# Kernel tuning notes

Hardware: AMD Instinct MI355X
Metric: run time of the kernel (lower is better)

Reference implementation:

```python
import jax, jax.numpy as jnp
import numpy as np

IN_CH = 1024
EMB = 1024
OUT = 768


def setup_inputs() -> dict:
    key = jax.random.key(0)
    ks = jax.random.split(key, 12)
    B, S = 8, 2048
    std = 1.0 / np.sqrt(IN_CH)
    return {
        "image_embeds": jax.random.normal(ks[0], (B, S, IN_CH), jnp.float32),
        "ref_pose_embeds": jax.random.normal(ks[1], (B, S, IN_CH), jnp.float32),
        "pose_embeds": jax.random.normal(ks[2], (B, S, IN_CH), jnp.float32),
        "ln_gamma": jnp.ones((IN_CH,), jnp.float32),
        "ln_beta": jnp.zeros((IN_CH,), jnp.float32),
        "Wq": jax.random.normal(ks[3], (EMB, IN_CH), jnp.float32) * std,
        "bq": jnp.zeros((EMB,), jnp.float32),
        "Wk": jax.random.normal(ks[4], (EMB, IN_CH), jnp.float32) * std,
        "bk": jnp.zeros((EMB,), jnp.float32),
        "Wv": jax.random.normal(ks[5], (EMB, IN_CH), jnp.float32) * std,
        "bv": jnp.zeros((EMB,), jnp.float32),
        "Wo": jax.random.normal(ks[6], (OUT, EMB), jnp.float32) * (1.0 / np.sqrt(EMB)),
        "bo": jnp.zeros((OUT,), jnp.float32),
    }


def _layernorm(x, gamma, beta, eps=1e-5):
    mu = jnp.mean(x, axis=-1, keepdims=True)
    var = jnp.var(x, axis=-1, keepdims=True)
    return (x - mu) * jax.lax.rsqrt(var + eps) * gamma + beta


def reference(image_embeds, ref_pose_embeds, pose_embeds,
              ln_gamma, ln_beta, Wq, bq, Wk, bk, Wv, bv, Wo, bo):
    scale = EMB ** (-0.5)
    # shared LayerNorm applied to all three streams (as in original)
    img_n = _layernorm(image_embeds, ln_gamma, ln_beta)
    ref_n = _layernorm(ref_pose_embeds, ln_gamma, ln_beta)
    pose_n = _layernorm(pose_embeds, ln_gamma, ln_beta)
    Q = ref_n @ Wq.T + bq   # [B,S,E]
    K = pose_n @ Wk.T + bk
    V = img_n @ Wv.T + bv
    att = jnp.einsum('bid,bjd->bij', Q, K) * scale  # [B,S,S]
    att = jax.nn.softmax(att, axis=-1)
    out = jnp.einsum('bij,bjd->bid', att, V)
    out = out + pose_n + img_n
    return out @ Wo.T + bo  # [B,S,768]
```

## Files before the change

### kernel.cpp

```cpp
#include <hip/hip_runtime.h>
#include <hip/hip_bf16.h>
#include <hip/hip_fp16.h>

typedef __attribute__((ext_vector_type(8))) short short8;
typedef __attribute__((ext_vector_type(4))) float f32x4;
typedef unsigned short u16;

__device__ __forceinline__ u16 f2bf(float f) {
  union { float f; unsigned u; } v; v.f = f;
  unsigned r = v.u + 0x7fffu + ((v.u >> 16) & 1u);
  return (u16)(r >> 16);
}
__device__ __forceinline__ float bf2f(u16 u) {
  union { unsigned u; float f; } v; v.u = ((unsigned)u) << 16;
  return v.f;
}
__device__ __forceinline__ u16 f2h(float f) {
  __half h = __float2half(f);
  union { __half h; u16 u; } v; v.h = h;
  return v.u;
}
__device__ __forceinline__ void gload16(const void* g, void* l) {
  __builtin_amdgcn_global_load_lds(
      (const __attribute__((address_space(1))) unsigned*)g,
      (__attribute__((address_space(3))) unsigned*)l, 16, 0, 0);
}

#define FENCE asm volatile("" ::: "memory")
#define SB0 __builtin_amdgcn_sched_barrier(0)

__global__ __launch_bounds__(256)
void ln3(const float* __restrict__ refp, const float* __restrict__ pose,
         const float* __restrict__ img, const float* __restrict__ gamma,
         const float* __restrict__ beta, u16* __restrict__ oA,
         u16* __restrict__ oB, u16* __restrict__ oC) {
  const int row = blockIdx.x;
  const int tid = threadIdx.x;
  const float* X = (blockIdx.y == 0) ? refp : (blockIdx.y == 1) ? pose : img;
  u16* Y = (blockIdx.y == 0) ? oA : (blockIdx.y == 1) ? oB : oC;
  const long base = (long)row * 1024 + tid * 4;
  float4 x = *(const float4*)(X + base);
  float s = x.x + x.y + x.z + x.w;
  float q = x.x * x.x + x.y * x.y + x.z * x.z + x.w * x.w;
#pragma unroll
  for (int o = 32; o > 0; o >>= 1) {
    s += __shfl_xor(s, o);
    q += __shfl_xor(q, o);
  }
  __shared__ float rs[4], rq[4];
  if ((tid & 63) == 0) { rs[tid >> 6] = s; rq[tid >> 6] = q; }
  __syncthreads();
  s = rs[0] + rs[1] + rs[2] + rs[3];
  q = rq[0] + rq[1] + rq[2] + rq[3];
  float mu = s * (1.f / 1024.f);
  float var = q * (1.f / 1024.f) - mu * mu;
  float rstd = rsqrtf(var + 1e-5f);
  float4 g = *(const float4*)(gamma + tid * 4);
  float4 b = *(const float4*)(beta + tid * 4);
  ushort4 o4;
  o4.x = f2bf((x.x - mu) * rstd * g.x + b.x);
  o4.y = f2bf((x.y - mu) * rstd * g.y + b.y);
  o4.z = f2bf((x.z - mu) * rstd * g.z + b.z);
  o4.w = f2bf((x.w - mu) * rstd * g.w + b.w);
  *(ushort4*)(Y + base) = o4;
}

__global__ __launch_bounds__(256)
void cvt_all(const float* __restrict__ Wq, const float* __restrict__ Wk,
             const float* __restrict__ Wv, const float* __restrict__ Wo,
             u16* __restrict__ oq, u16* __restrict__ ok, u16* __restrict__ ov,
             u16* __restrict__ oo) {
  int i = blockIdx.x * 256 + threadIdx.x;
  const int W1 = 262144;
  const float* src;
  u16* dst;
  int j;
  if (i < W1) { src = Wq; dst = oq; j = i; }
  else if (i < 2 * W1) { src = Wk; dst = ok; j = i - W1; }
  else if (i < 3 * W1) { src = Wv; dst = ov; j = i - 2 * W1; }
  else { src = Wo; dst = oo; j = i - 3 * W1; }
  float4 x = ((const float4*)src)[j];
  ushort4 o;
  o.x = f2bf(x.x); o.y = f2bf(x.y); o.z = f2bf(x.z); o.w = f2bf(x.w);
  ((ushort4*)dst)[j] = o;
}

__global__ __launch_bounds__(256)
void softmax_inplace(u16* __restrict__ LP) {
  const int tid = threadIdx.x;
  const long base = (long)blockIdx.x * 2048 + tid * 8;
  const __half* hp = (const __half*)LP + base;
  short8 raw = *(const short8*)hp;
  float x[8];
#pragma unroll
  for (int i = 0; i < 8; ++i) x[i] = __half2float(((const __half*)&raw)[i]);
  float m = x[0];
#pragma unroll
  for (int i = 1; i < 8; ++i) m = fmaxf(m, x[i]);
#pragma unroll
  for (int o = 32; o > 0; o >>= 1) m = fmaxf(m, __shfl_xor(m, o));
  __shared__ float red[8];
  if ((tid & 63) == 0) red[tid >> 6] = m;
  __syncthreads();
  m = fmaxf(fmaxf(red[0], red[1]), fmaxf(red[2], red[3]));
  float e[8];
  float s = 0.f;
#pragma unroll
  for (int i = 0; i < 8; ++i) { e[i] = __expf(x[i] - m); s += e[i]; }
#pragma unroll
  for (int o = 32; o > 0; o >>= 1) s += __shfl_xor(s, o);
  if ((tid & 63) == 0) red[4 + (tid >> 6)] = s;
  __syncthreads();
  s = red[4] + red[5] + red[6] + red[7];
  float inv = 1.f / s;
  short8 out;
#pragma unroll
  for (int i = 0; i < 8; ++i) ((u16*)&out)[i] = f2bf(e[i] * inv);
  *(short8*)((__half*)LP + base) = out;
}

template <int MODE>
__global__ __launch_bounds__(512, 2)
void gemm256(const u16* __restrict__ A, const u16* __restrict__ B,
             const float* __restrict__ bias, void* __restrict__ Cp,
             const u16* __restrict__ R1, const u16* __restrict__ R2,
             int M, int N, int K, long sA, long sB, long sC, float scale,
             int ntx, int nty, int g, int fdim) {
  extern __shared__ char lds[];
  const int nwg = gridDim.x;
  const int chunk = nwg >> 3;
  int l = (blockIdx.x & 7) * chunk + (blockIdx.x >> 3);
  const int per = ntx * nty;
  const int tz = l / per;
  int li = l - tz * per;
  const int ns = fdim ? nty : ntx;
  const int fi = li % g;
  const int s_ = (li / g) % ns;
  const int fB = li / (g * ns);
  const int f = fB * g + fi;
  const int tx = fdim ? f : s_;
  const int ty = fdim ? s_ : f;

  const u16* Ab = A + (long)tz * sA;
  const u16* Bb = B + (long)tz * sB;
  const long cb = (long)tz * sC;

  const int tid = threadIdx.x;
  const int lane = tid & 63;
  const int wid = tid >> 6;
  const int wr = wid >> 2;
  const int wc = wid & 3;
  const long rowBase = (long)ty * 256;
  const long colBase = (long)tx * 256;
  const int fr = lane & 15;
  const int fk = lane >> 4;
  const int nt = K >> 6;

  auto stage = [&](const u16* __restrict__ gb, long rcBase, int t, int h, int bOff) {
    char* base = lds + (t & 1) * 65536 + bOff + h * 16384;
    const long kk = (long)t << 6;
#pragma unroll
    for (int i = 0; i < 2; ++i) {
      const int o = i * 8192 + tid * 16;
      const int row = o >> 7;
      const int cs = (o >> 4) & 7;
      const long gr = rcBase + h * 128 + row;
      const long gk = kk + (long)((cs ^ (row & 7)) << 3);
      gload16(gb + gr * (long)K + gk, base + o);
    }
  };

  auto ldA = [&](int t, int m, int ks) -> short8 {
    const int row = wr * 128 + m * 16 + fr;
    const int ch = (ks * 4 + fk) ^ (row & 7);
    return *(const short8*)(lds + (t & 1) * 65536 + row * 128 + ch * 16);
  };
  auto ldB = [&](int t, int n, int ks) -> short8 {
    const int row = wc * 64 + n * 16 + fr;
    const int ch = (ks * 4 + fk) ^ (row & 7);
    return *(const short8*)(lds + (t & 1) * 65536 + 32768 + row * 128 + ch * 16);
  };

  f32x4 acc[8][4] = {};
  short8 ar[4][2];
  short8 br[4][2];

  stage(Ab, rowBase, 0, 0, 0);
  stage(Ab, rowBase, 0, 1, 0);
  stage(Bb, colBase, 0, 0, 32768);
  stage(Bb, colBase, 0, 1, 32768);
  if (nt > 1) {
    stage(Ab, rowBase, 1, 0, 0);
    stage(Bb, colBase, 1, 0, 32768);
    stage(Bb, colBase, 1, 1, 32768);
    asm volatile("s_waitcnt vmcnt(6)" ::: "memory");
  } else {
    asm volatile("s_waitcnt vmcnt(0)" ::: "memory");
  }
  FENCE; __builtin_amdgcn_s_barrier(); FENCE;

#define MFMA16(MB, NB)                                                               \
  __builtin_amdgcn_s_setprio(1);                                                     \
  _Pragma("unroll") for (int k2 = 0; k2 < 2; ++k2)                                   \
  _Pragma("unroll") for (int nn = 0; nn < 2; ++nn)                                   \
  _Pragma("unroll") for (int mm = 0; mm < 4; ++mm)                                   \
      acc[(MB) + mm][(NB) + nn] = __builtin_amdgcn_mfma_f32_16x16x32_bf16(           \
          ar[mm][k2], br[(NB) + nn][k2], acc[(MB) + mm][(NB) + nn], 0, 0, 0);        \
  __builtin_amdgcn_s_setprio(0);

  for (int t = 0; t < nt; ++t) {
#pragma unroll
    for (int mm = 0; mm < 4; ++mm) { ar[mm][0] = ldA(t, mm, 0); ar[mm][1] = ldA(t, mm, 1); }
#pragma unroll
    for (int nn = 0; nn < 2; ++nn) { br[nn][0] = ldB(t, nn, 0); br[nn][1] = ldB(t, nn, 1); }
    if (t + 1 < nt) stage(Ab, rowBase, t + 1, 1, 0);
    FENCE; __builtin_amdgcn_s_barrier(); FENCE; SB0;
    MFMA16(0, 0);
    SB0; FENCE; __builtin_amdgcn_s_barrier(); FENCE;

#pragma unroll
    for (int nn = 2; nn < 4; ++nn) { br[nn][0] = ldB(t, nn, 0); br[nn][1] = ldB(t, nn, 1); }
    FENCE; __builtin_amdgcn_s_barrier(); FENCE; SB0;
    MFMA16(0, 2);
    SB0; FENCE; __builtin_amdgcn_s_barrier(); FENCE;

#pragma unroll
    for (int mm = 0; mm < 4; ++mm) { ar[mm][0] = ldA(t, 4 + mm, 0); ar[mm][1] = ldA(t, 4 + mm, 1); }
    if (t + 2 < nt) stage(Bb, colBase, t + 2, 0, 32768);
    FENCE; __builtin_amdgcn_s_barrier(); FENCE; SB0;
    MFMA16(4, 0);
    SB0; FENCE; __builtin_amdgcn_s_barrier(); FENCE;

    if (t + 2 < nt) {
      stage(Bb, colBase, t + 2, 1, 32768);
      stage(Ab, rowBase, t + 2, 0, 0);
      asm volatile("s_waitcnt vmcnt(6)" ::: "memory");
    } else {
      asm volatile("s_waitcnt vmcnt(0)" ::: "memory");
    }
    FENCE; __builtin_amdgcn_s_barrier(); FENCE; SB0;
    MFMA16(4, 2);
    SB0; FENCE; __builtin_amdgcn_s_barrier(); FENCE;
  }
#undef MFMA16

#pragma unroll
  for (int m = 0; m < 8; ++m) {
#pragma unroll
    for (int n = 0; n < 4; ++n) {
      const long r = rowBase + wr * 128 + m * 16 + fk * 4;
      const long c = colBase + wc * 64 + n * 16 + fr;
      f32x4 v = acc[m][n];
      if (MODE == 0) {
        float4 bb = *(const float4*)(bias + r);
        ushort4 o;
        o.x = f2bf(v[0] + bb.x); o.y = f2bf(v[1] + bb.y);
        o.z = f2bf(v[2] + bb.z); o.w = f2bf(v[3] + bb.w);
        *(ushort4*)((u16*)Cp + c * (long)M + r) = o;
      } else if (MODE == 1) {
        ushort4 o;
        o.x = f2h(v[0] * scale); o.y = f2h(v[1] * scale);
        o.z = f2h(v[2] * scale); o.w = f2h(v[3] * scale);
        *(ushort4*)((u16*)Cp + cb + c * (long)M + r) = o;
      } else if (MODE == 2) {
        const long b2 = r >> 11;
        const long i = r & 2047;
        const float bc = bias[c];
        ushort4 o;
        o.x = f2bf(v[0] + bc); o.y = f2bf(v[1] + bc);
        o.z = f2bf(v[2] + bc); o.w = f2bf(v[3] + bc);
        *(ushort4*)((u16*)Cp + b2 * 2097152L + c * 2048L + i) = o;
      } else if (MODE == 3) {
        const long idx = cb + c * (long)M + r;
        ushort4 r1 = *(const ushort4*)(R1 + idx);
        ushort4 r2 = *(const ushort4*)(R2 + idx);
        ushort4 o;
        o.x = f2bf(v[0] + bf2f(r1.x) + bf2f(r2.x));
        o.y = f2bf(v[1] + bf2f(r1.y) + bf2f(r2.y));
        o.z = f2bf(v[2] + bf2f(r1.z) + bf2f(r2.z));
        o.w = f2bf(v[3] + bf2f(r1.w) + bf2f(r2.w));
        *(ushort4*)((u16*)Cp + idx) = o;
      } else {
        float4 bb = *(const float4*)(bias + r);
        float4 o;
        o.x = v[0] + bb.x; o.y = v[1] + bb.y; o.z = v[2] + bb.z; o.w = v[3] + bb.w;
        *(float4*)((float*)Cp + c * (long)M + r) = o;
      }
    }
  }
}

extern "C" void kernel_launch(void* const* d_in, const int* in_sizes, int n_in,
                              void* d_out, int out_size, void* d_ws, size_t ws_size,
                              hipStream_t stream) {
  const float* img  = (const float*)d_in[0];
  const float* refp = (const float*)d_in[1];
  const float* pose = (const float*)d_in[2];
  const float* gam  = (const float*)d_in[3];
  const float* bet  = (const float*)d_in[4];
  const float* Wq = (const float*)d_in[5];
  const float* bq = (const float*)d_in[6];
  const float* Wk = (const float*)d_in[7];
  const float* bk = (const float*)d_in[8];
  const float* Wv = (const float*)d_in[9];
  const float* bv = (const float*)d_in[10];
  const float* Wo = (const float*)d_in[11];
  const float* bo = (const float*)d_in[12];

  char* ws = (char*)d_ws;
  const size_t MB = 1u << 20;
  u16* Wq_b = (u16*)(ws + 0 * MB);
  u16* Wk_b = (u16*)(ws + 2 * MB);
  u16* Wv_b = (u16*)(ws + 4 * MB);
  u16* Wo_b = (u16*)(ws + 6 * MB);
  u16* bufA = (u16*)(ws + 8 * MB);
  u16* bufB = (u16*)(ws + 40 * MB);
  u16* bufC = (u16*)(ws + 72 * MB);
  u16* bufD = (u16*)(ws + 104 * MB);
  u16* bufE = (u16*)(ws + 136 * MB);
  u16* bufL = (u16*)(ws + 168 * MB);

  const int LDSB = 131072;
  hipFuncSetAttribute((const void*)gemm256<0>, hipFuncAttributeMaxDynamicSharedMemorySize, LDSB);
  hipFuncSetAttribute((const void*)gemm256<1>, hipFuncAttributeMaxDynamicSharedMemorySize, LDSB);
  hipFuncSetAttribute((const void*)gemm256<2>, hipFuncAttributeMaxDynamicSharedMemorySize, LDSB);
  hipFuncSetAttribute((const void*)gemm256<3>, hipFuncAttributeMaxDynamicSharedMemorySize, LDSB);
  hipFuncSetAttribute((const void*)gemm256<4>, hipFuncAttributeMaxDynamicSharedMemorySize, LDSB);

  cvt_all<<<3840, 256, 0, stream>>>(Wq, Wk, Wv, Wo, Wq_b, Wk_b, Wv_b, Wo_b);

  ln3<<<dim3(16384, 3), 256, 0, stream>>>(refp, pose, img, gam, bet, bufA, bufB, bufC);

  gemm256<0><<<256, 512, LDSB, stream>>>(Wq_b, bufA, bq, bufD, nullptr, nullptr,
                                         1024, 16384, 1024, 0, 0, 0, 1.f,
                                         64, 4, 4, 0);
  gemm256<0><<<256, 512, LDSB, stream>>>(Wk_b, bufB, bk, bufA, nullptr, nullptr,
                                         1024, 16384, 1024, 0, 0, 0, 1.f,
                                         64, 4, 4, 0);
  gemm256<2><<<256, 512, LDSB, stream>>>(bufC, Wv_b, bv, bufE, nullptr, nullptr,
                                         16384, 1024, 1024, 0, 0, 0, 1.f,
                                         4, 64, 4, 1);
  gemm256<1><<<512, 512, LDSB, stream>>>(bufA, bufD, nullptr, bufL, nullptr, nullptr,
                                         2048, 2048, 1024,
                                         2048L * 1024, 2048L * 1024, 2048L * 2048,
                                         0.03125f, 8, 8, 4, 0);
  softmax_inplace<<<16384, 256, 0, stream>>>(bufL);
  gemm256<3><<<256, 512, LDSB, stream>>>(bufE, bufL, nullptr, bufD, bufB, bufC,
                                         1024, 2048, 2048,
                                         1024L * 2048, 2048L * 2048, 2048L * 1024, 1.f,
                                         8, 4, 4, 0);
  gemm256<4><<<192, 512, LDSB, stream>>>(Wo_b, bufD, bo, d_out, nullptr, nullptr,
                                         768, 16384, 1024, 0, 0, 0, 1.f,
                                         64, 3, 3, 0);
}
```

Before: 410.8 us.

## Fuse softmax into QK and PV GEMM epilogues with atomic row sums

Removes the separate softmax pass. The QK^T GEMM epilogue now writes exp(scaled score) in bf16 and atomically accumulates per-row sums, and the PV GEMM epilogue normalizes by those sums before adding the residuals. This avoids an extra read and write of the full attention matrix, at the cost of dropping max subtraction, which could overflow for large scores. The GEMM main loop is also unrolled over both LDS buffers with precomputed swizzled offsets to cut address arithmetic.

```diff
diff --git a/kernel.cpp b/kernel.cpp
--- a/kernel.cpp
+++ b/kernel.cpp
@@ -1,6 +1,5 @@
 #include <hip/hip_runtime.h>
 #include <hip/hip_bf16.h>
-#include <hip/hip_fp16.h>
 
 typedef __attribute__((ext_vector_type(8))) short short8;
 typedef __attribute__((ext_vector_type(4))) float f32x4;
@@ -15,11 +14,6 @@
   union { unsigned u; float f; } v; v.u = ((unsigned)u) << 16;
   return v.f;
 }
-__device__ __forceinline__ u16 f2h(float f) {
-  __half h = __float2half(f);
-  union { __half h; u16 u; } v; v.h = h;
-  return v.u;
-}
 __device__ __forceinline__ void gload16(const void* g, void* l) {
   __builtin_amdgcn_global_load_lds(
       (const __attribute__((address_space(1))) unsigned*)g,
@@ -28,6 +22,7 @@
 
 #define FENCE asm volatile("" ::: "memory")
 #define SB0 __builtin_amdgcn_sched_barrier(0)
+#define BAR do { FENCE; __builtin_amdgcn_s_barrier(); FENCE; } while (0)
 
 __global__ __launch_bounds__(256)
 void ln3(const float* __restrict__ refp, const float* __restrict__ pose,
@@ -85,45 +80,12 @@
   ((ushort4*)dst)[j] = o;
 }
 
-__global__ __launch_bounds__(256)
-void softmax_inplace(u16* __restrict__ LP) {
-  const int tid = threadIdx.x;
-  const long base = (long)blockIdx.x * 2048 + tid * 8;
-  const __half* hp = (const __half*)LP + base;
-  short8 raw = *(const short8*)hp;
-  float x[8];
-#pragma unroll
-  for (int i = 0; i < 8; ++i) x[i] = __half2float(((const __half*)&raw)[i]);
-  float m = x[0];
-#pragma unroll
-  for (int i = 1; i < 8; ++i) m = fmaxf(m, x[i]);
-#pragma unroll
-  for (int o = 32; o > 0; o >>= 1) m = fmaxf(m, __shfl_xor(m, o));
-  __shared__ float red[8];
-  if ((tid & 63) == 0) red[tid >> 6] = m;
-  __syncthreads();
-  m = fmaxf(fmaxf(red[0], red[1]), fmaxf(red[2], red[3]));
-  float e[8];
-  float s = 0.f;
-#pragma unroll
-  for (int i = 0; i < 8; ++i) { e[i] = __expf(x[i] - m); s += e[i]; }
-#pragma unroll
-  for (int o = 32; o > 0; o >>= 1) s += __shfl_xor(s, o);
-  if ((tid & 63) == 0) red[4 + (tid >> 6)] = s;
-  __syncthreads();
-  s = red[4] + red[5] + red[6] + red[7];
-  float inv = 1.f / s;
-  short8 out;
-#pragma unroll
-  for (int i = 0; i < 8; ++i) ((u16*)&out)[i] = f2bf(e[i] * inv);
-  *(short8*)((__half*)LP + base) = out;
-}
-
 template <int MODE>
 __global__ __launch_bounds__(512, 2)
 void gemm256(const u16* __restrict__ A, const u16* __restrict__ B,
              const float* __restrict__ bias, void* __restrict__ Cp,
              const u16* __restrict__ R1, const u16* __restrict__ R2,
+             float* __restrict__ rsum,
              int M, int N, int K, long sA, long sB, long sC, float scale,
              int ntx, int nty, int g, int fdim) {
   extern __shared__ char lds[];
@@ -136,8 +98,8 @@
   const int ns = fdim ? nty : ntx;
   const int fi = li % g;
   const int s_ = (li / g) % ns;
-  const int fB = li / (g * ns);
-  const int f = fB * g + fi;
+  const int fB2 = li / (g * ns);
+  const int f = fB2 * g + fi;
   const int tx = fdim ? f : s_;
   const int ty = fdim ? s_ : f;
 
@@ -156,8 +118,18 @@
   const int fk = lane >> 4;
   const int nt = K >> 6;
 
-  auto stage = [&](const u16* __restrict__ gb, long rcBase, int t, int h, int bOff) {
-    char* base = lds + (t & 1) * 65536 + bOff + h * 16384;
+  const int ch0 = (fk ^ (fr & 7)) * 16;
+  const int ch1 = ((4 + fk) ^ (fr & 7)) * 16;
+  const int aB = (wr * 128 + fr) * 128;
+  const int bB = 32768 + (wc * 64 + fr) * 128;
+
+#define LDA(BUF, m, k2) \
+  (*(const short8*)(lds + (BUF) * 65536 + aB + (m) * 2048 + ((k2) ? ch1 : ch0)))
+#define LDB(BUF, n, k2) \
+  (*(const short8*)(lds + (BUF) * 65536 + bB + (n) * 2048 + ((k2) ? ch1 : ch0)))
+
+  auto stage = [&](const u16* __restrict__ gb, long rcBase, int t, int h, int bOff, int buf) {
+    char* base = lds + buf * 65536 + bOff + h * 16384;
     const long kk = (long)t << 6;
 #pragma unroll
     for (int i = 0; i < 2; ++i) {
@@ -170,124 +142,146 @@
     }
   };
 
-  auto ldA = [&](int t, int m, int ks) -> short8 {
-    const int row = wr * 128 + m * 16 + fr;
-    const int ch = (ks * 4 + fk) ^ (row & 7);
-    return *(const short8*)(lds + (t & 1) * 65536 + row * 128 + ch * 16);
-  };
-  auto ldB = [&](int t, int n, int ks) -> short8 {
-    const int row = wc * 64 + n * 16 + fr;
-    const int ch = (ks * 4 + fk) ^ (row & 7);
-    return *(const short8*)(lds + (t & 1) * 65536 + 32768 + row * 128 + ch * 16);
-  };
-
   f32x4 acc[8][4] = {};
   short8 ar[4][2];
   short8 br[4][2];
 
-  stage(Ab, rowBase, 0, 0, 0);
-  stage(Ab, rowBase, 0, 1, 0);
-  stage(Bb, colBase, 0, 0, 32768);
-  stage(Bb, colBase, 0, 1, 32768);
-  if (nt > 1) {
-    stage(Ab, rowBase, 1, 0, 0);
-    stage(Bb, colBase, 1, 0, 32768);
-    stage(Bb, colBase, 1, 1, 32768);
-    asm volatile("s_waitcnt vmcnt(6)" ::: "memory");
-  } else {
-    asm volatile("s_waitcnt vmcnt(0)" ::: "memory");
-  }
-  FENCE; __builtin_amdgcn_s_barrier(); FENCE;
-
-#define MFMA16(MB, NB)                                                               \
+#define RDA(BUF, M0)                                         \
+  _Pragma("unroll") for (int mm = 0; mm < 4; ++mm) {         \
+    ar[mm][0] = LDA(BUF, (M0) + mm, 0);                      \
+    ar[mm][1] = LDA(BUF, (M0) + mm, 1);                      \
+  }
+#define RDB2(BUF, N0)                                        \
+  _Pragma("unroll") for (int nn = 0; nn < 2; ++nn) {         \
+    br[(N0) + nn][0] = LDB(BUF, (N0) + nn, 0);               \
+    br[(N0) + nn][1] = LDB(BUF, (N0) + nn, 1);               \
+  }
+#define MFMAQ(M0, N0)                                                                \
   __builtin_amdgcn_s_setprio(1);                                                     \
   _Pragma("unroll") for (int k2 = 0; k2 < 2; ++k2)                                   \
   _Pragma("unroll") for (int nn = 0; nn < 2; ++nn)                                   \
   _Pragma("unroll") for (int mm = 0; mm < 4; ++mm)                                   \
-      acc[(MB) + mm][(NB) + nn] = __builtin_amdgcn_mfma_f32_16x16x32_bf16(           \
-          ar[mm][k2], br[(NB) + nn][k2], acc[(MB) + mm][(NB) + nn], 0, 0, 0);        \
+      acc[(M0) + mm][(N0) + nn] = __builtin_amdgcn_mfma_f32_16x16x32_bf16(           \
+          ar[mm][k2], br[(N0) + nn][k2], acc[(M0) + mm][(N0) + nn], 0, 0, 0);        \
   __builtin_amdgcn_s_setprio(0);
 
-  for (int t = 0; t < nt; ++t) {
-#pragma unroll
-    for (int mm = 0; mm < 4; ++mm) { ar[mm][0] = ldA(t, mm, 0); ar[mm][1] = ldA(t, mm, 1); }
-#pragma unroll
-    for (int nn = 0; nn < 2; ++nn) { br[nn][0] = ldB(t, nn, 0); br[nn][1] = ldB(t, nn, 1); }
-    if (t + 1 < nt) stage(Ab, rowBase, t + 1, 1, 0);
-    FENCE; __builtin_amdgcn_s_barrier(); FENCE; SB0;
-    MFMA16(0, 0);
-    SB0; FENCE; __builtin_amdgcn_s_barrier(); FENCE;
-
-#pragma unroll
-    for (int nn = 2; nn < 4; ++nn) { br[nn][0] = ldB(t, nn, 0); br[nn][1] = ldB(t, nn, 1); }
-    FENCE; __builtin_amdgcn_s_barrier(); FENCE; SB0;
-    MFMA16(0, 2);
-    SB0; FENCE; __builtin_amdgcn_s_barrier(); FENCE;
-
-#pragma unroll
-    for (int mm = 0; mm < 4; ++mm) { ar[mm][0] = ldA(t, 4 + mm, 0); ar[mm][1] = ldA(t, 4 + mm, 1); }
-    if (t + 2 < nt) stage(Bb, colBase, t + 2, 0, 32768);
-    FENCE; __builtin_amdgcn_s_barrier(); FENCE; SB0;
-    MFMA16(4, 0);
-    SB0; FENCE; __builtin_amdgcn_s_barrier(); FENCE;
-
-    if (t + 2 < nt) {
-      stage(Bb, colBase, t + 2, 1, 32768);
-      stage(Ab, rowBase, t + 2, 0, 0);
-      asm volatile("s_waitcnt vmcnt(6)" ::: "memory");
-    } else {
-      asm volatile("s_waitcnt vmcnt(0)" ::: "memory");
+#define GTILE(T, BUF)                                                      \
+  do {                                                                     \
+    RDA(BUF, 0);                                                           \
+    RDB2(BUF, 0);                                                          \
+    if ((T) + 1 < nt) stage(Ab, rowBase, (T) + 1, 1, 0, (BUF) ^ 1);        \
+    BAR; SB0; MFMAQ(0, 0); SB0; BAR;                                       \
+    RDB2(BUF, 2);                                                          \
+    BAR; SB0; MFMAQ(0, 2); SB0; BAR;                                       \
+    RDA(BUF, 4);                                                           \
+    if ((T) + 2 < nt) stage(Bb, colBase, (T) + 2, 0, 32768, BUF);          \
+    BAR; SB0; MFMAQ(4, 0); SB0; BAR;                                       \
+    if ((T) + 2 < nt) {                                                    \
+      stage(Bb, colBase, (T) + 2, 1, 32768, BUF);                          \
+      stage(Ab, rowBase, (T) + 2, 0, 0, BUF);                              \
+      asm volatile("s_waitcnt vmcnt(6)" ::: "memory");                     \
+    } else {                                                               \
+      asm volatile("s_waitcnt vmcnt(0)" ::: "memory");                     \
+    }                                                                      \
+    BAR; SB0; MFMAQ(4, 2); SB0; BAR;                                       \
+  } while (0)
+
+  stage(Ab, rowBase, 0, 0, 0, 0);
+  stage(Ab, rowBase, 0, 1, 0, 0);
+  stage(Bb, colBase, 0, 0, 32768, 0);
+  stage(Bb, colBase, 0, 1, 32768, 0);
+  if (nt > 1) {
+    stage(Ab, rowBase, 1, 0, 0, 1);
+    stage(Bb, colBase, 1, 0, 32768, 1);
+    stage(Bb, colBase, 1, 1, 32768, 1);
+    asm volatile("s_waitcnt vmcnt(6)" ::: "memory");
+  } else {
+    asm volatile("s_waitcnt vmcnt(0)" ::: "memory");
+  }
+  BAR;
+
+  for (int tt = 0; tt < nt; tt += 2) {
+    GTILE(tt, 0);
+    GTILE(tt + 1, 1);
+  }
+
+  if (MODE == 1) {
+#pragma unroll
+    for (int n = 0; n < 4; ++n) {
+      const long c = colBase + wc * 64 + n * 16 + fr;
+      float ps = 0.f;
+#pragma unroll
+      for (int m = 0; m < 8; ++m) {
+        const long r = rowBase + wr * 128 + m * 16 + fk * 4;
+        f32x4 v = acc[m][n];
+        float e0 = __expf(v[0] * scale), e1 = __expf(v[1] * scale);
+        float e2 = __expf(v[2] * scale), e3 = __expf(v[3] * scale);
+        ps += (e0 + e1) + (e2 + e3);
+        ushort4 o;
+        o.x = f2bf(e0); o.y = f2bf(e1); o.z = f2bf(e2); o.w = f2bf(e3);
+        *(ushort4*)((u16*)Cp + cb + c * (long)M + r) = o;
+      }
+      ps += __shfl_xor(ps, 16);
+      ps += __shfl_xor(ps, 32);
+      if (lane < 16) atomicAdd(&rsum[(long)tz * 2048 + c], ps);
     }
-    FENCE; __builtin_amdgcn_s_barrier(); FENCE; SB0;
-    MFMA16(4, 2);
-    SB0; FENCE; __builtin_amdgcn_s_barrier(); FENCE;
-  }
-#undef MFMA16
-
-#pragma unroll
-  for (int m = 0; m < 8; ++m) {
+  } else if (MODE == 3) {
 #pragma unroll
     for (int n = 0; n < 4; ++n) {
-      const long r = rowBase + wr * 128 + m * 16 + fk * 4;
       const long c = colBase + wc * 64 + n * 16 + fr;
-      f32x4 v = acc[m][n];
-      if (MODE == 0) {
-        float4 bb = *(const float4*)(bias + r);
-        ushort4 o;
-        o.x = f2bf(v[0] + bb.x); o.y = f2bf(v[1] + bb.y);
-        o.z = f2bf(v[2] + bb.z); o.w = f2bf(v[3] + bb.w);
-        *(ushort4*)((u16*)Cp + c * (long)M + r) = o;
-      } else if (MODE == 1) {
-        ushort4 o;
-        o.x = f2h(v[0] * scale); o.y = f2h(v[1] * scale);
-        o.z = f2h(v[2] * scale); o.w = f2h(v[3] * scale);
-        *(ushort4*)((u16*)Cp + cb + c * (long)M + r) = o;
-      } else if (MODE == 2) {
-        const long b2 = r >> 11;
-        const long i = r & 2047;
-        const float bc = bias[c];
-        ushort4 o;
-        o.x = f2bf(v[0] + bc); o.y = f2bf(v[1] + bc);
-        o.z = f2bf(v[2] + bc); o.w = f2bf(v[3] + bc);
-        *(ushort4*)((u16*)Cp + b2 * 2097152L + c * 2048L + i) = o;
-      } else if (MODE == 3) {
+      const float inv = 1.f / rsum[(long)tz * 2048 + c];
+#pragma unroll
+      for (int m = 0; m < 8; ++m) {
+        const long r = rowBase + wr * 128 + m * 16 + fk * 4;
         const long idx = cb + c * (long)M + r;
+        f32x4 v = acc[m][n];
         ushort4 r1 = *(const ushort4*)(R1 + idx);
         ushort4 r2 = *(const ushort4*)(R2 + idx);
         ushort4 o;
-        o.x = f2bf(v[0] + bf2f(r1.x) + bf2f(r2.x));
-        o.y = f2bf(v[1] + bf2f(r1.y) + bf2f(r2.y));
-        o.z = f2bf(v[2] + bf2f(r1.z) + bf2f(r2.z));
-        o.w = f2bf(v[3] + bf2f(r1.w) + bf2f(r2.w));
+        o.x = f2bf(v[0] * inv + bf2f(r1.x) + bf2f(r2.x));
+        o.y = f2bf(v[1] * inv + bf2f(r1.y) + bf2f(r2.y));
+        o.z = f2bf(v[2] * inv + bf2f(r1.z) + bf2f(r2.z));
+        o.w = f2bf(v[3] * inv + bf2f(r1.w) + bf2f(r2.w));
         *(ushort4*)((u16*)Cp + idx) = o;
-      } else {
-        float4 bb = *(const float4*)(bias + r);
-        float4 o;
-        o.x = v[0] + bb.x; o.y = v[1] + bb.y; o.z = v[2] + bb.z; o.w = v[3] + bb.w;
-        *(float4*)((float*)Cp + c * (long)M + r) = o;
       }
     }
-  }
+  } else {
+#pragma unroll
+    for (int m = 0; m < 8; ++m) {
+#pragma unroll
+      for (int n = 0; n < 4; ++n) {
+        const long r = rowBase + wr * 128 + m * 16 + fk * 4;
+        const long c = colBase + wc * 64 + n * 16 + fr;
+        f32x4 v = acc[m][n];
+        if (MODE == 0) {
+          float4 bb = *(const float4*)(bias + r);
+          ushort4 o;
+          o.x = f2bf(v[0] + bb.x); o.y = f2bf(v[1] + bb.y);
+          o.z = f2bf(v[2] + bb.z); o.w = f2bf(v[3] + bb.w);
+          *(ushort4*)((u16*)Cp + c * (long)M + r) = o;
+        } else if (MODE == 2) {
+          const long b2 = r >> 11;
+          const long i = r & 2047;
+          const float bc = bias[c];
+          ushort4 o;
+          o.x = f2bf(v[0] + bc); o.y = f2bf(v[1] + bc);
+          o.z = f2bf(v[2] + bc); o.w = f2bf(v[3] + bc);
+          *(ushort4*)((u16*)Cp + b2 * 2097152L + c * 2048L + i) = o;
+        } else {
+          float4 bb = *(const float4*)(bias + r);
+          float4 o;
+          o.x = v[0] + bb.x; o.y = v[1] + bb.y; o.z = v[2] + bb.z; o.w = v[3] + bb.w;
+          *(float4*)((float*)Cp + c * (long)M + r) = o;
+        }
+      }
+    }
+  }
+#undef LDA
+#undef LDB
+#undef RDA
+#undef RDB2
+#undef MFMAQ
+#undef GTILE
 }
 
 extern "C" void kernel_launch(void* const* d_in, const int* in_sizes, int n_in,
@@ -313,6 +307,7 @@
   u16* Wk_b = (u16*)(ws + 2 * MB);
   u16* Wv_b = (u16*)(ws + 4 * MB);
   u16* Wo_b = (u16*)(ws + 6 * MB);
+  float* rowsum = (float*)(ws + 7 * MB + 512 * 1024);
   u16* bufA = (u16*)(ws + 8 * MB);
   u16* bufB = (u16*)(ws + 40 * MB);
   u16* bufC = (u16*)(ws + 72 * MB);
@@ -327,29 +322,30 @@
   hipFuncSetAttribute((const void*)gemm256<3>, hipFuncAttributeMaxDynamicSharedMemorySize, LDSB);
   hipFuncSetAttribute((const void*)gemm256<4>, hipFuncAttributeMaxDynamicSharedMemorySize, LDSB);
 
+  hipMemsetAsync(rowsum, 0, 8 * 2048 * sizeof(float), stream);
+
   cvt_all<<<3840, 256, 0, stream>>>(Wq, Wk, Wv, Wo, Wq_b, Wk_b, Wv_b, Wo_b);
 
   ln3<<<dim3(16384, 3), 256, 0, stream>>>(refp, pose, img, gam, bet, bufA, bufB, bufC);
 
-  gemm256<0><<<256, 512, LDSB, stream>>>(Wq_b, bufA, bq, bufD, nullptr, nullptr,
+  gemm256<0><<<256, 512, LDSB, stream>>>(Wq_b, bufA, bq, bufD, nullptr, nullptr, nullptr,
                                          1024, 16384, 1024, 0, 0, 0, 1.f,
                                          64, 4, 4, 0);
-  gemm256<0><<<256, 512, LDSB, stream>>>(Wk_b, bufB, bk, bufA, nullptr, nullptr,
+  gemm256<0><<<256, 512, LDSB, stream>>>(Wk_b, bufB, bk, bufA, nullptr, nullptr, nullptr,
                                          1024, 16384, 1024, 0, 0, 0, 1.f,
                                          64, 4, 4, 0);
-  gemm256<2><<<256, 512, LDSB, stream>>>(bufC, Wv_b, bv, bufE, nullptr, nullptr,
+  gemm256<2><<<256, 512, LDSB, stream>>>(bufC, Wv_b, bv, bufE, nullptr, nullptr, nullptr,
                                          16384, 1024, 1024, 0, 0, 0, 1.f,
                                          4, 64, 4, 1);
-  gemm256<1><<<512, 512, LDSB, stream>>>(bufA, bufD, nullptr, bufL, nullptr, nullptr,
+  gemm256<1><<<512, 512, LDSB, stream>>>(bufA, bufD, nullptr, bufL, nullptr, nullptr, rowsum,
                                          2048, 2048, 1024,
                                          2048L * 1024, 2048L * 1024, 2048L * 2048,
                                          0.03125f, 8, 8, 4, 0);
-  softmax_inplace<<<16384, 256, 0, stream>>>(bufL);
-  gemm256<3><<<256, 512, LDSB, stream>>>(bufE, bufL, nullptr, bufD, bufB, bufC,
+  gemm256<3><<<256, 512, LDSB, stream>>>(bufE, bufL, nullptr, bufD, bufB, bufC, rowsum,
                                          1024, 2048, 2048,
                                          1024L * 2048, 2048L * 2048, 2048L * 1024, 1.f,
                                          8, 4, 4, 0);
-  gemm256<4><<<192, 512, LDSB, stream>>>(Wo_b, bufD, bo, d_out, nullptr, nullptr,
+  gemm256<4><<<192, 512, LDSB, stream>>>(Wo_b, bufD, bo, d_out, nullptr, nullptr, nullptr,
                                          768, 16384, 1024, 0, 0, 0, 1.f,
                                          64, 3, 3, 0);
 }
```

After: 392.5 us. 4.5% less time.
